# Kernel tuning notes

Measured on AMD Instinct MI355X. Metric: run time of the kernel, lower is better.

## Reference

```python
import jax, jax.numpy as jnp
import numpy as np

U2 = 1024          # unit2
DIM = 3 * U2       # input_dim == units == 3072
BATCH = 16384


def _build_mask(rng: np.random.Generator) -> np.ndarray:
    """Reconstruct the STN block-structured binary mask, shape (units, input_dim).

    Row blocks (units) x col blocks (inputs), each U2 x U2:
      rows [0,U2):      [ones,        Bern(1/2), zeros     ]
      rows [U2,2U2):    [Bern(1/2),   Bern(3/4), Bern(1/2) ]
      rows [2U2,3U2):   [zeros,       Bern(1/2), ones      ]
    """
    def bern(p, shape):
        return (rng.random(shape) < p).astype(np.float32)
    ones = np.ones((U2, U2), np.float32)
    zeros = np.zeros((U2, U2), np.float32)
    row1 = np.concatenate([ones, bern(0.5, (U2, U2)), zeros], axis=1)
    row2 = np.concatenate([bern(0.5, (U2, U2)), bern(0.75, (U2, U2)), bern(0.5, (U2, U2))], axis=1)
    row3 = np.concatenate([zeros, bern(0.5, (U2, U2)), ones], axis=1)
    return np.concatenate([row1, row2, row3], axis=0)


def setup_inputs() -> dict:
    key = jax.random.key(0)
    kx, kw = jax.random.split(key)
    x = jax.random.normal(kx, (BATCH, DIM), dtype=jnp.float32)
    # w init: uniform [0, 0.01], non-negative constraint holds at init
    w = jax.random.uniform(kw, (DIM, DIM), dtype=jnp.float32, minval=0.0, maxval=0.01)
    b = jnp.zeros((DIM,), dtype=jnp.float32)  # stn_bias = [0, 0]
    mask = jnp.asarray(_build_mask(np.random.default_rng(0)))
    return {"x": x, "w": w, "b": b, "mask": mask}


def reference(x, w, b, mask):
    # Original: p = transpose(s @ x^T) -> (B, units, dim); f = diag_part(p @ w) + b
    # Algebraic identity: f[b,u] = b[u] + sum_d mask[u,d] * x[b,d] * w[d,u]
    # i.e. a dense matmul against the masked weight W_eff[d,u] = mask[u,d] * w[d,u].
    w_eff = mask.T * w                     # (dim, units)
    return x @ w_eff + b                   # (batch, units)
```

## Files before the change

kernel.cpp:

```cpp
#include <hip/hip_runtime.h>
#include <hip/hip_bf16.h>
#include <stdint.h>

#define DIM   3072
#define BATCH 16384

typedef __attribute__((ext_vector_type(8))) short bf16x8;
typedef __attribute__((ext_vector_type(4))) float f32x4;

__device__ __forceinline__ unsigned short f2b(float f) {
    union { float f; unsigned u; } c; c.f = f;
    unsigned u = c.u;
    unsigned r = (u + 0x7fffu + ((u >> 16) & 1u)) >> 16;
    return (unsigned short)r;
}

#define NWT   2304
#define NCVT  2048
__global__ __launch_bounds__(256) void prep_kernel(const float* __restrict__ w,
                                                   const float* __restrict__ mask,
                                                   const float* __restrict__ x,
                                                   ushort* __restrict__ wt,
                                                   ushort* __restrict__ xb) {
    if (blockIdx.x < NWT) {
        __shared__ float tile[64][65];
        const int u0 = (blockIdx.x % 48) * 64;
        const int d0 = (blockIdx.x / 48) * 64;
        const int t  = threadIdx.x;
        const int rr = t >> 4, cc = t & 15;
#pragma unroll
        for (int it = 0; it < 4; ++it) {
            int drow = it * 16 + rr;
            float4 v = *reinterpret_cast<const float4*>(&w[(size_t)(d0 + drow) * DIM + u0 + cc * 4]);
            tile[drow][cc * 4 + 0] = v.x;
            tile[drow][cc * 4 + 1] = v.y;
            tile[drow][cc * 4 + 2] = v.z;
            tile[drow][cc * 4 + 3] = v.w;
        }
        __syncthreads();
#pragma unroll
        for (int it = 0; it < 4; ++it) {
            int urow = it * 16 + rr;
            float4 mv = *reinterpret_cast<const float4*>(&mask[(size_t)(u0 + urow) * DIM + d0 + cc * 4]);
            ushort4 o;
            o.x = f2b(tile[cc * 4 + 0][urow] * mv.x);
            o.y = f2b(tile[cc * 4 + 1][urow] * mv.y);
            o.z = f2b(tile[cc * 4 + 2][urow] * mv.z);
            o.w = f2b(tile[cc * 4 + 3][urow] * mv.w);
            *reinterpret_cast<ushort4*>(&wt[(size_t)(u0 + urow) * DIM + d0 + cc * 4]) = o;
        }
    } else {
        const int n4 = BATCH * DIM / 4;
        const int stride = NCVT * 256;
        for (int i = (blockIdx.x - NWT) * 256 + threadIdx.x; i < n4; i += stride) {
            float4 v = reinterpret_cast<const float4*>(x)[i];
            ushort4 o;
            o.x = f2b(v.x); o.y = f2b(v.y); o.z = f2b(v.z); o.w = f2b(v.w);
            reinterpret_cast<ushort4*>(xb)[i] = o;
        }
    }
}

#define GLOAD_LDS16(g, l)                                                                 \
    __builtin_amdgcn_global_load_lds((const __attribute__((address_space(1))) void*)(g),  \
                                     (__attribute__((address_space(3))) void*)(l), 16, 0, 0)

__global__ __launch_bounds__(512, 1) void gemm8p(const ushort* __restrict__ A,
                                                 const ushort* __restrict__ B,
                                                 const float* __restrict__ bias,
                                                 float* __restrict__ C) {
    __shared__ ushort sh[2 * 2 * 16384];

    const int tid  = threadIdx.x;
    const int lane = tid & 63;
    const int wid  = tid >> 6;
    const int wr   = wid >> 2;
    const int wc   = wid & 3;
    const int l15  = lane & 15;
    const int kg   = lane >> 4;
    const int sx   = lane & 7;

    const int srow = lane >> 3;
    const int sg   = (lane & 7) ^ srow;

    const int orig = blockIdx.x;
    const int wg   = (orig & 7) * (gridDim.x >> 3) + (orig >> 3);
    const int tm   = wg / 12;
    const int tn   = wg - tm * 12;
    const int brow = tm * 256, bcol = tn * 256;

    f32x4 acc[8][4] = {};
    bf16x8 a_[8], b0_[4], b1_[4];

#define STAGE(b, side, h, tt)                                                              \
    do {                                                                                   \
        int _t = (tt) < 47 ? (tt) : 47;                                                    \
        const ushort* _base = (side) ? B : A;                                              \
        int _r0 = ((side) ? bcol : brow) + (h) * 128 + wid * 16 + srow;                    \
        const ushort* _g0 = _base + (size_t)_r0 * DIM + _t * 64 + sg * 8;                  \
        ushort* _l0 = sh + ((b) * 2 + (side)) * 16384 + (h) * 8192 + wid * 1024;           \
        GLOAD_LDS16(_g0, _l0);                                                             \
        GLOAD_LDS16(_g0 + (size_t)8 * DIM, _l0 + 512);                                     \
    } while (0)

#define LDA(QB, QM)                                                                        \
    _Pragma("unroll") for (int fm = 0; fm < 4; ++fm)                                       \
    _Pragma("unroll") for (int ks = 0; ks < 2; ++ks)                                       \
        a_[fm * 2 + ks] = *reinterpret_cast<const bf16x8*>(                                \
            sh + (QB) * 32768 + (wr * 128 + (QM) * 64 + fm * 16 + l15) * 64 +              \
            (((ks * 4 + kg) ^ sx) * 8));

#define LDB(DST, QB, QN)                                                                   \
    _Pragma("unroll") for (int fn = 0; fn < 2; ++fn)                                       \
    _Pragma("unroll") for (int ks = 0; ks < 2; ++ks)                                       \
        DST[fn * 2 + ks] = *reinterpret_cast<const bf16x8*>(                               \
            sh + (QB) * 32768 + 16384 + (wc * 64 + (QN) * 32 + fn * 16 + l15) * 64 +       \
            (((ks * 4 + kg) ^ sx) * 8));

#define MMQ(QM, QN, BARR)                                                                  \
    _Pragma("unroll") for (int fm = 0; fm < 4; ++fm)                                       \
    _Pragma("unroll") for (int fn = 0; fn < 2; ++fn)                                       \
    _Pragma("unroll") for (int ks = 0; ks < 2; ++ks)                                       \
        acc[(QM) * 4 + fm][(QN) * 2 + fn] = __builtin_amdgcn_mfma_f32_16x16x32_bf16(       \
            a_[fm * 2 + ks], BARR[fn * 2 + ks], acc[(QM) * 4 + fm][(QN) * 2 + fn], 0, 0, 0);

#define MIDSYNC()                                                                          \
    __builtin_amdgcn_s_barrier();                                                          \
    asm volatile("s_waitcnt lgkmcnt(0)" ::: "memory");                                     \
    __builtin_amdgcn_sched_barrier(0);                                                     \
    __builtin_amdgcn_s_setprio(1);

#define ENDPHASE()                                                                         \
    __builtin_amdgcn_s_setprio(0);                                                         \
    __builtin_amdgcn_s_barrier();

    STAGE(0, 0, 0, 0);
    STAGE(0, 0, 1, 0);
    STAGE(0, 1, 0, 0);
    STAGE(0, 1, 1, 0);
    STAGE(1, 1, 0, 1);
    STAGE(1, 1, 1, 1);
    asm volatile("s_waitcnt vmcnt(4)" ::: "memory");
    __builtin_amdgcn_s_barrier();

    for (int t = 0; t < 48; t += 2) {
        LDA(0, 0); LDB(b0_, 0, 0);
        STAGE(1, 0, 0, t + 1);
        MIDSYNC(); MMQ(0, 0, b0_); ENDPHASE();
        LDB(b1_, 0, 1);
        STAGE(1, 0, 1, t + 1);
        MIDSYNC(); MMQ(0, 1, b1_); ENDPHASE();
        LDA(0, 1);
        STAGE(0, 1, 0, t + 2);
        MIDSYNC(); MMQ(1, 0, b0_); ENDPHASE();
        STAGE(0, 1, 1, t + 2);
        asm volatile("s_waitcnt vmcnt(4)" ::: "memory");
        MIDSYNC(); MMQ(1, 1, b1_); ENDPHASE();
        LDA(1, 0); LDB(b0_, 1, 0);
        STAGE(0, 0, 0, t + 2);
        MIDSYNC(); MMQ(0, 0, b0_); ENDPHASE();
        LDB(b1_, 1, 1);
        STAGE(0, 0, 1, t + 2);
        MIDSYNC(); MMQ(0, 1, b1_); ENDPHASE();
        LDA(1, 1);
        STAGE(1, 1, 0, t + 3);
        MIDSYNC(); MMQ(1, 0, b0_); ENDPHASE();
        STAGE(1, 1, 1, t + 3);
        asm volatile("s_waitcnt vmcnt(4)" ::: "memory");
        MIDSYNC(); MMQ(1, 1, b1_); ENDPHASE();
    }

#pragma unroll
    for (int n = 0; n < 4; ++n) {
        int col = bcol + wc * 64 + n * 16 + l15;
        float bv = bias[col];
#pragma unroll
        for (int m = 0; m < 8; ++m) {
            int row0 = brow + wr * 128 + m * 16 + kg * 4;
#pragma unroll
            for (int r = 0; r < 4; ++r)
                C[(size_t)(row0 + r) * DIM + col] = acc[m][n][r] + bv;
        }
    }
#undef STAGE
#undef LDA
#undef LDB
#undef MMQ
#undef MIDSYNC
#undef ENDPHASE
}

extern "C" void kernel_launch(void* const* d_in, const int* in_sizes, int n_in,
                              void* d_out, int out_size, void* d_ws, size_t ws_size,
                              hipStream_t stream) {
    const float* x    = (const float*)d_in[0];
    const float* w    = (const float*)d_in[1];
    const float* bias = (const float*)d_in[2];
    const float* mask = (const float*)d_in[3];
    float* out = (float*)d_out;

    const size_t wt_bytes = (size_t)DIM * DIM * sizeof(ushort);
    const size_t xb_off   = (wt_bytes + 255) & ~(size_t)255;

    ushort* wt = (ushort*)d_ws;
    ushort* xb = (ushort*)((char*)d_ws + xb_off);

    prep_kernel<<<NWT + NCVT, 256, 0, stream>>>(w, mask, x, wt, xb);
    gemm8p<<<(BATCH / 256) * (DIM / 256), 512, 0, stream>>>(xb, wt, bias, out);
}
```

Before: 347.6 us.

## Make GEMM persistent with 256 blocks each processing three tiles with cross-tile prefetch

```diff
diff --git a/kernel.cpp b/kernel.cpp
--- a/kernel.cpp
+++ b/kernel.cpp
@@ -83,20 +83,23 @@
     const int srow = lane >> 3;
     const int sg   = (lane & 7) ^ srow;
 
-    const int orig = blockIdx.x;
-    const int wg   = (orig & 7) * (gridDim.x >> 3) + (orig >> 3);
-    const int tm   = wg / 12;
-    const int tn   = wg - tm * 12;
-    const int brow = tm * 256, bcol = tn * 256;
+    const int bx  = blockIdx.x;
+    const int xcd = bx & 7, loc = bx >> 3;
+    int q    = xcd * 96 + loc;
+    int brow = (q / 12) * 256, bcol = (q % 12) * 256;
+    int nrow = brow, ncol = bcol, nvalid = 0;
 
     f32x4 acc[8][4] = {};
     bf16x8 a_[8], b0_[4], b1_[4];
+    const f32x4 fzero = {};
 
 #define STAGE(b, side, h, tt)                                                              \
     do {                                                                                   \
-        int _t = (tt) < 47 ? (tt) : 47;                                                    \
+        int _tt = (tt);                                                                    \
+        int _t  = (_tt < 48) ? _tt : (nvalid ? _tt - 48 : 47);                             \
+        int _rb = (_tt < 48) ? ((side) ? bcol : brow) : ((side) ? ncol : nrow);            \
         const ushort* _base = (side) ? B : A;                                              \
-        int _r0 = ((side) ? bcol : brow) + (h) * 128 + wid * 16 + srow;                    \
+        int _r0 = _rb + (h) * 128 + wid * 16 + srow;                                       \
         const ushort* _g0 = _base + (size_t)_r0 * DIM + _t * 64 + sg * 8;                  \
         ushort* _l0 = sh + ((b) * 2 + (side)) * 16384 + (h) * 8192 + wid * 1024;           \
         GLOAD_LDS16(_g0, _l0);                                                             \
@@ -143,44 +146,62 @@
     asm volatile("s_waitcnt vmcnt(4)" ::: "memory");
     __builtin_amdgcn_s_barrier();
 
-    for (int t = 0; t < 48; t += 2) {
-        LDA(0, 0); LDB(b0_, 0, 0);
-        STAGE(1, 0, 0, t + 1);
-        MIDSYNC(); MMQ(0, 0, b0_); ENDPHASE();
-        LDB(b1_, 0, 1);
-        STAGE(1, 0, 1, t + 1);
-        MIDSYNC(); MMQ(0, 1, b1_); ENDPHASE();
-        LDA(0, 1);
-        STAGE(0, 1, 0, t + 2);
-        MIDSYNC(); MMQ(1, 0, b0_); ENDPHASE();
-        STAGE(0, 1, 1, t + 2);
-        asm volatile("s_waitcnt vmcnt(4)" ::: "memory");
-        MIDSYNC(); MMQ(1, 1, b1_); ENDPHASE();
-        LDA(1, 0); LDB(b0_, 1, 0);
-        STAGE(0, 0, 0, t + 2);
-        MIDSYNC(); MMQ(0, 0, b0_); ENDPHASE();
-        LDB(b1_, 1, 1);
-        STAGE(0, 0, 1, t + 2);
-        MIDSYNC(); MMQ(0, 1, b1_); ENDPHASE();
-        LDA(1, 1);
-        STAGE(1, 1, 0, t + 3);
-        MIDSYNC(); MMQ(1, 0, b0_); ENDPHASE();
-        STAGE(1, 1, 1, t + 3);
-        asm volatile("s_waitcnt vmcnt(4)" ::: "memory");
-        MIDSYNC(); MMQ(1, 1, b1_); ENDPHASE();
-    }
-
-#pragma unroll
-    for (int n = 0; n < 4; ++n) {
-        int col = bcol + wc * 64 + n * 16 + l15;
-        float bv = bias[col];
-#pragma unroll
-        for (int m = 0; m < 8; ++m) {
-            int row0 = brow + wr * 128 + m * 16 + kg * 4;
-#pragma unroll
-            for (int r = 0; r < 4; ++r)
-                C[(size_t)(row0 + r) * DIM + col] = acc[m][n][r] + bv;
-        }
+    for (int r = 0; r < 3; ++r) {
+        nvalid = (r < 2);
+        int qn = nvalid ? (xcd * 96 + (r + 1) * 32 + loc) : q;
+        nrow = (qn / 12) * 256;
+        ncol = (qn % 12) * 256;
+
+        float bv[4];
+#pragma unroll
+        for (int n = 0; n < 4; ++n) bv[n] = bias[bcol + wc * 64 + n * 16 + l15];
+
+        for (int t = 0; t < 48; t += 2) {
+            LDA(0, 0); LDB(b0_, 0, 0);
+            STAGE(1, 0, 0, t + 1);
+            MIDSYNC(); MMQ(0, 0, b0_); ENDPHASE();
+            LDB(b1_, 0, 1);
+            STAGE(1, 0, 1, t + 1);
+            MIDSYNC(); MMQ(0, 1, b1_); ENDPHASE();
+            LDA(0, 1);
+            STAGE(0, 1, 0, t + 2);
+            MIDSYNC(); MMQ(1, 0, b0_); ENDPHASE();
+            STAGE(0, 1, 1, t + 2);
+            asm volatile("s_waitcnt vmcnt(4)" ::: "memory");
+            MIDSYNC(); MMQ(1, 1, b1_); ENDPHASE();
+            LDA(1, 0); LDB(b0_, 1, 0);
+            STAGE(0, 0, 0, t + 2);
+            MIDSYNC(); MMQ(0, 0, b0_); ENDPHASE();
+            LDB(b1_, 1, 1);
+            STAGE(0, 0, 1, t + 2);
+            MIDSYNC(); MMQ(0, 1, b1_); ENDPHASE();
+            LDA(1, 1);
+            STAGE(1, 1, 0, t + 3);
+            MIDSYNC(); MMQ(1, 0, b0_); ENDPHASE();
+            STAGE(1, 1, 1, t + 3);
+            asm volatile("s_waitcnt vmcnt(4)" ::: "memory");
+            MIDSYNC(); MMQ(1, 1, b1_); ENDPHASE();
+        }
+
+#pragma unroll
+        for (int n = 0; n < 4; ++n) {
+            int col = bcol + wc * 64 + n * 16 + l15;
+#pragma unroll
+            for (int m = 0; m < 8; ++m) {
+                int row0 = brow + wr * 128 + m * 16 + kg * 4;
+#pragma unroll
+                for (int rr = 0; rr < 4; ++rr)
+                    C[(size_t)(row0 + rr) * DIM + col] = acc[m][n][rr] + bv[n];
+            }
+        }
+        if (r < 2) {
+#pragma unroll
+            for (int m = 0; m < 8; ++m)
+#pragma unroll
+                for (int n = 0; n < 4; ++n)
+                    acc[m][n] = fzero;
+        }
+        q = qn; brow = nrow; bcol = ncol;
     }
 #undef STAGE
 #undef LDA
@@ -206,5 +227,5 @@
     ushort* xb = (ushort*)((char*)d_ws + xb_off);
 
     prep_kernel<<<NWT + NCVT, 256, 0, stream>>>(w, mask, x, wt, xb);
-    gemm8p<<<(BATCH / 256) * (DIM / 256), 512, 0, stream>>>(xb, wt, bias, out);
-}
+    gemm8p<<<256, 512, 0, stream>>>(xb, wt, bias, out);
+}
```

Result: faster. 340.7 us (median of 2 runs) (-2.0%).
